# Kernel tuning notes

Measured on AMD Instinct MI355X. Metric: run time of the kernel, lower is better.

Reference implementation:

```python
import jax, jax.numpy as jnp
import numpy as np

N = 60000          # users
M = 40000          # items
NODES = N + M
D = 64             # embedding_dim
NLAYERS = 3        # layers = [64, 64, 64]
NNZ = 3_200_000    # nnz of L_I (avg degree 32)
B = 1024           # batch_size
NEG_SLOPE = 0.2


def setup_inputs() -> dict:
    key = jax.random.key(0)
    ks = jax.random.split(key, 12)
    edge_row = jax.random.randint(ks[0], (NNZ,), 0, NODES, dtype=jnp.int32)
    edge_col = jax.random.randint(ks[1], (NNZ,), 0, NODES, dtype=jnp.int32)
    # Laplacian values are small positive normalized weights
    edge_val = jax.random.uniform(ks[2], (NNZ,), dtype=jnp.float32) * (1.0 / 32.0)
    embed_user = jax.random.normal(ks[3], (N, D), dtype=jnp.float32) * 0.1
    embed_item = jax.random.normal(ks[4], (M, D), dtype=jnp.float32) * 0.1
    W1 = jax.random.normal(ks[5], (NLAYERS, D, D), dtype=jnp.float32) * 0.1
    W2 = jax.random.normal(ks[6], (NLAYERS, D, D), dtype=jnp.float32) * 0.1
    b1 = jax.random.normal(ks[7], (NLAYERS, 1, D), dtype=jnp.float32) * 0.1
    b2 = jax.random.normal(ks[8], (NLAYERS, 1, D), dtype=jnp.float32) * 0.1
    sampled_users = jax.random.randint(ks[9], (B,), 0, N, dtype=jnp.int32)
    observed_items_idx = jax.random.randint(ks[10], (B,), 0, M, dtype=jnp.int32)
    unobserved_items_idx = jax.random.randint(ks[11], (B,), 0, M, dtype=jnp.int32)
    return {
        "edge_row": edge_row, "edge_col": edge_col, "edge_val": edge_val,
        "embed_user": embed_user, "embed_item": embed_item,
        "W1": W1, "W2": W2, "b1": b1, "b2": b2,
        "sampled_users": sampled_users,
        "observed_items_idx": observed_items_idx,
        "unobserved_items_idx": unobserved_items_idx,
    }


def _spmm(row, col, val, x):
    # sparse (NODES x NODES) @ dense (NODES x D) via gather + segment-sum
    return jax.ops.segment_sum(val[:, None] * x[col], row, num_segments=NODES)


def reference(edge_row, edge_col, edge_val, embed_user, embed_item,
              W1, W2, b1, b2,
              sampled_users, observed_items_idx, unobserved_items_idx):
    x = jnp.concatenate([embed_user, embed_item], axis=0)  # (NODES, D)
    reprs = [x]
    for i in range(NLAYERS):
        lie = _spmm(edge_row, edge_col, edge_val, x)        # L_I @ E
        left = lie @ W1[i] + b1[i]
        right = (x * lie) @ W2[i] + b2[i]
        x = jax.nn.leaky_relu(left + right, negative_slope=NEG_SLOPE)
        reprs.append(x)
    final_reprs = jnp.concatenate(reprs, axis=1)            # (NODES, D*(NLAYERS+1))
    users_, items_ = final_reprs[:N], final_reprs[N:]
    return (users_[sampled_users],
            items_[observed_items_idx],
            items_[unobserved_items_idx])
```

## Files before the change

kernel.cpp:

```cpp
#include <hip/hip_runtime.h>

#define NN    60000
#define NODES 100000
#define DD    64
#define NNZ   3200000
#define BB    1024
#define NEG   0.2f
#define RPB   196
#define NBUCK 511
#define EPB   8192
#define NPB   ((NNZ + EPB - 1) / EPB)
#define CAP   7000
#define BCAP  7168
#define NSEG  13
#define KEYN  (NSEG * RPB)
#define SPB   (KEYN + 1)

__global__ __launch_bounds__(256) void k_init_x(const float* __restrict__ eu,
                                                const float* __restrict__ ei,
                                                float* __restrict__ x,
                                                int* __restrict__ gcur) {
    int i = blockIdx.x * 256 + threadIdx.x;
    if (i < NBUCK) gcur[i] = i * CAP;
    const int TOT = NODES * DD / 4;
    if (i >= TOT) return;
    const int UE = NN * DD / 4;
    float4 v = (i < UE) ? ((const float4*)eu)[i] : ((const float4*)ei)[i - UE];
    ((float4*)x)[i] = v;
}

__global__ __launch_bounds__(512) void k_place(const int* __restrict__ row,
                                               const int* __restrict__ col,
                                               const float* __restrict__ val,
                                               int* __restrict__ gcur,
                                               int2* __restrict__ bulk) {
    __shared__ int rows_l[EPB];
    __shared__ unsigned short perm[EPB];
    __shared__ int h[NBUCK], bloc[NBUCK], bcur[NBUCK], gseg[NBUCK];
    __shared__ int sc[512];
    int t = threadIdx.x;
    if (t < NBUCK) h[t] = 0;
    __syncthreads();
    int base = blockIdx.x * EPB;
    int n = min(EPB, NNZ - base);
    for (int k = t; k < n; k += 512) {
        int r = row[base + k];
        rows_l[k] = r;
        atomicAdd(&h[r / RPB], 1);
    }
    __syncthreads();
    {
        int v = (t < NBUCK) ? h[t] : 0;
        sc[t] = v;
        __syncthreads();
        for (int off = 1; off < 512; off <<= 1) {
            int u = (t >= off) ? sc[t - off] : 0;
            __syncthreads();
            sc[t] += u;
            __syncthreads();
        }
        if (t < NBUCK) {
            int ex = sc[t] - v;
            bloc[t] = ex;
            bcur[t] = ex;
            gseg[t] = v ? atomicAdd(&gcur[t], v) : 0;
        }
    }
    __syncthreads();
    for (int k = t; k < n; k += 512) {
        int p = atomicAdd(&bcur[rows_l[k] / RPB], 1);
        perm[p] = (unsigned short)k;
    }
    __syncthreads();
    for (int j = t; j < n; j += 512) {
        int k = perm[j];
        int r = rows_l[k];
        int b = r / RPB;
        int addr = gseg[b] + (j - bloc[b]);
        bulk[addr] = make_int2(((r - b * RPB) << 17) | col[base + k],
                               __float_as_int(val[base + k]));
    }
}

__global__ __launch_bounds__(512) void k_csr(const int* __restrict__ gcur,
                                             int2* __restrict__ bulk,
                                             int* __restrict__ starts) {
    __shared__ int2 eds[BCAP];
    __shared__ int cnt[KEYN], pos[KEYN];
    __shared__ int part[512];
    int b = blockIdx.x, t = threadIdx.x;
    int lo = b * CAP;
    int n = gcur[b] - lo;
    for (int k = t; k < KEYN; k += 512) cnt[k] = 0;
    __syncthreads();
    for (int i = t; i < n; i += 512) {
        int2 ed = bulk[lo + i];
        eds[i] = ed;
        int lr = ed.x >> 17, c = ed.x & 0x1FFFF;
        atomicAdd(&cnt[(c >> 13) * RPB + lr], 1);
    }
    __syncthreads();
    int run = 0;
#pragma unroll
    for (int j = 0; j < 5; ++j) {
        int k = t * 5 + j;
        if (k < KEYN) { pos[k] = run; run += cnt[k]; }
    }
    part[t] = run;
    __syncthreads();
    for (int off = 1; off < 512; off <<= 1) {
        int u = (t >= off) ? part[t - off] : 0;
        __syncthreads();
        part[t] += u;
        __syncthreads();
    }
    int poff = part[t] - run;
#pragma unroll
    for (int j = 0; j < 5; ++j) {
        int k = t * 5 + j;
        if (k < KEYN) pos[k] += poff;
    }
    __syncthreads();
    for (int k = t; k < KEYN; k += 512) {
        starts[b * SPB + k] = lo + pos[k];
        cnt[k] = pos[k];
    }
    if (t == 0) starts[b * SPB + KEYN] = lo + n;
    __syncthreads();
    for (int i = t; i < n; i += 512) {
        int2 ed = eds[i];
        int lr = ed.x >> 17, c = ed.x & 0x1FFFF;
        int p = atomicAdd(&cnt[(c >> 13) * RPB + lr], 1);
        bulk[lo + p] = ed;
    }
}

__global__ __launch_bounds__(1024) void k_cspmm(const int* __restrict__ starts,
                                                const int2* __restrict__ cv,
                                                const float* __restrict__ x,
                                                float* __restrict__ lie) {
    __shared__ float acc[RPB * DD];
    int t = threadIdx.x, b = blockIdx.x;
    float4* av = (float4*)acc;
    for (int i = t; i < RPB * 16; i += 1024) av[i] = make_float4(0.f, 0.f, 0.f, 0.f);
    __syncthreads();
    int lane = t & 63;
    int wid = __builtin_amdgcn_readfirstlane(t >> 6);
    int r0 = (wid * RPB) >> 4;
    int r1 = ((wid + 1) * RPB) >> 4;
    int sb = b * SPB;
    for (int seg = 0; seg < NSEG; ++seg) {
        int s = starts[sb + seg * RPB + r0];
        int e = starts[sb + seg * RPB + r1];
        int cur = -1;
        float f = 0.f;
        int g = s;
        for (; g + 8 <= e; g += 8) {
            int2 ee[8];
#pragma unroll
            for (int j = 0; j < 8; ++j) ee[j] = cv[g + j];
            float xv[8];
#pragma unroll
            for (int j = 0; j < 8; ++j) xv[j] = x[(ee[j].x & 0x1FFFF) * DD + lane];
#pragma unroll
            for (int j = 0; j < 8; ++j) {
                int r = ee[j].x >> 17;
                if (r != cur) {
                    if (cur >= 0) acc[cur * DD + lane] += f;
                    cur = r; f = 0.f;
                }
                f = fmaf(__int_as_float(ee[j].y), xv[j], f);
            }
        }
        for (; g < e; ++g) {
            int2 ed = cv[g];
            float xg = x[(ed.x & 0x1FFFF) * DD + lane];
            int r = ed.x >> 17;
            if (r != cur) {
                if (cur >= 0) acc[cur * DD + lane] += f;
                cur = r; f = 0.f;
            }
            f = fmaf(__int_as_float(ed.y), xg, f);
        }
        if (cur >= 0) acc[cur * DD + lane] += f;
    }
    __syncthreads();
    int row0 = b * RPB;
    for (int i = t; i < RPB * 16; i += 1024) {
        int gr = row0 + (i >> 4);
        if (gr < NODES) ((float4*)lie)[gr * 16 + (i & 15)] = av[i];
    }
}

__global__ __launch_bounds__(256) void k_gemm(float* __restrict__ x,
                                              const float* __restrict__ lie,
                                              const float* __restrict__ W1,
                                              const float* __restrict__ W2,
                                              const float* __restrict__ b1,
                                              const float* __restrict__ b2) {
    __shared__ float A1[64 * 64];
    __shared__ float A2[64 * 64];
    __shared__ float Ws1[64 * 64];
    __shared__ float Ws2[64 * 64];

    const int t = threadIdx.x;
    const int row0 = blockIdx.x * 64;

    {
        const float4* w1v = (const float4*)W1;
        const float4* w2v = (const float4*)W2;
        float4* s1v = (float4*)Ws1;
        float4* s2v = (float4*)Ws2;
#pragma unroll
        for (int q = 0; q < 4; ++q) {
            s1v[q * 256 + t] = w1v[q * 256 + t];
            s2v[q * 256 + t] = w2v[q * 256 + t];
        }
    }
#pragma unroll
    for (int q = 0; q < 4; ++q) {
        int f4 = q * 256 + t;
        int rl = f4 >> 4;
        int c4 = f4 & 15;
        int gr = row0 + rl;
        float4 lv = make_float4(0.f, 0.f, 0.f, 0.f);
        float4 xv = make_float4(0.f, 0.f, 0.f, 0.f);
        if (gr < NODES) {
            lv = *(const float4*)&lie[gr * DD + c4 * 4];
            xv = *(const float4*)&x[gr * DD + c4 * 4];
        }
        int sg = c4 ^ (rl & 15);
        ((float4*)A1)[rl * 16 + sg] = lv;
        ((float4*)A2)[rl * 16 + sg] = make_float4(lv.x * xv.x, lv.y * xv.y,
                                                  lv.z * xv.z, lv.w * xv.w);
    }
    __syncthreads();

    const int tx = t & 15;
    const int ty = t >> 4;
    float bs[4];
    {
        float4 bb1 = *(const float4*)&b1[tx * 4];
        float4 bb2 = *(const float4*)&b2[tx * 4];
        bs[0] = bb1.x + bb2.x; bs[1] = bb1.y + bb2.y;
        bs[2] = bb1.z + bb2.z; bs[3] = bb1.w + bb2.w;
    }
    float acc[4][4];
#pragma unroll
    for (int i = 0; i < 4; ++i)
#pragma unroll
        for (int j = 0; j < 4; ++j) acc[i][j] = bs[j];

    for (int k4 = 0; k4 < 16; ++k4) {
        float4 a1[4], a2[4];
#pragma unroll
        for (int i = 0; i < 4; ++i) {
            int r = ty * 4 + i;
            int sg = k4 ^ (r & 15);
            a1[i] = ((const float4*)A1)[r * 16 + sg];
            a2[i] = ((const float4*)A2)[r * 16 + sg];
        }
#pragma unroll
        for (int kk = 0; kk < 4; ++kk) {
            float4 w1 = ((const float4*)Ws1)[(k4 * 4 + kk) * 16 + tx];
            float4 w2 = ((const float4*)Ws2)[(k4 * 4 + kk) * 16 + tx];
#pragma unroll
            for (int i = 0; i < 4; ++i) {
                float av1 = (&a1[i].x)[kk];
                float av2 = (&a2[i].x)[kk];
                acc[i][0] = fmaf(av1, w1.x, fmaf(av2, w2.x, acc[i][0]));
                acc[i][1] = fmaf(av1, w1.y, fmaf(av2, w2.y, acc[i][1]));
                acc[i][2] = fmaf(av1, w1.z, fmaf(av2, w2.z, acc[i][2]));
                acc[i][3] = fmaf(av1, w1.w, fmaf(av2, w2.w, acc[i][3]));
            }
        }
    }
#pragma unroll
    for (int i = 0; i < 4; ++i) {
        int gr = row0 + ty * 4 + i;
        if (gr < NODES) {
            float4 o;
            o.x = acc[i][0] >= 0.f ? acc[i][0] : NEG * acc[i][0];
            o.y = acc[i][1] >= 0.f ? acc[i][1] : NEG * acc[i][1];
            o.z = acc[i][2] >= 0.f ? acc[i][2] : NEG * acc[i][2];
            o.w = acc[i][3] >= 0.f ? acc[i][3] : NEG * acc[i][3];
            *(float4*)&x[gr * DD + tx * 4] = o;
        }
    }
}

__global__ __launch_bounds__(256) void k_gather(const float* __restrict__ x,
                                                const int* __restrict__ su,
                                                const int* __restrict__ oi,
                                                const int* __restrict__ ui,
                                                float* __restrict__ out, int layer) {
    int w    = (blockIdx.x * 256 + threadIdx.x) >> 6;
    int lane = threadIdx.x & 63;
    if (w >= 3 * BB) return;
    int g = w >> 10, b = w & 1023;
    int node = (g == 0) ? su[b] : (NN + ((g == 1) ? oi[b] : ui[b]));
    out[w * 256 + layer * 64 + lane] = x[node * DD + lane];
}

extern "C" void kernel_launch(void* const* d_in, const int* in_sizes, int n_in,
                              void* d_out, int out_size, void* d_ws, size_t ws_size,
                              hipStream_t stream) {
    const int*   edge_row = (const int*)d_in[0];
    const int*   edge_col = (const int*)d_in[1];
    const float* edge_val = (const float*)d_in[2];
    const float* eu = (const float*)d_in[3];
    const float* ei = (const float*)d_in[4];
    const float* W1 = (const float*)d_in[5];
    const float* W2 = (const float*)d_in[6];
    const float* b1 = (const float*)d_in[7];
    const float* b2 = (const float*)d_in[8];
    const int*   su = (const int*)d_in[9];
    const int*   oi = (const int*)d_in[10];
    const int*   ui = (const int*)d_in[11];
    float* out = (float*)d_out;

    float* x      = (float*)d_ws;
    float* lie    = x + NODES * DD;
    int2*  bulk   = (int2*)(lie + NODES * DD);
    int*   gcur   = (int*)(bulk + NBUCK * CAP);
    int*   starts = gcur + NBUCK + 1;

    k_init_x<<<(NODES * DD / 4 + 255) / 256, 256, 0, stream>>>(eu, ei, x, gcur);
    k_gather<<<(3 * BB * 64 + 255) / 256, 256, 0, stream>>>(x, su, oi, ui, out, 0);

    k_place<<<NPB, 512, 0, stream>>>(edge_row, edge_col, edge_val, gcur, bulk);
    k_csr<<<NBUCK, 512, 0, stream>>>(gcur, bulk, starts);

    for (int l = 0; l < 3; ++l) {
        k_cspmm<<<NBUCK, 1024, 0, stream>>>(starts, bulk, x, lie);
        k_gemm<<<(NODES + 63) / 64, 256, 0, stream>>>(x, lie,
                                                      W1 + l * 4096, W2 + l * 4096,
                                                      b1 + l * 64,  b2 + l * 64);
        k_gather<<<(3 * BB * 64 + 255) / 256, 256, 0, stream>>>(x, su, oi, ui, out, l + 1);
    }
}
```

Baseline: 524.2 us.

## Fuse SpMM with dense layer transform, ping-pong x buffers, software-pipeline gathers

Adds a fused kernel that keeps each block's L·E rows in shared memory and applies the W1/W2 transform, bias and leaky ReLU directly, skipping the intermediate lie write and re-read. x is now double-buffered so the fused kernel can read the old x while writing the new one. The SpMM inner loop is software-pipelined across two register sets so the next batch's edge loads and x gathers are issued before the current batch is consumed. Layer 1 still uses the separate SpMM plus GEMM path. The fused GEMM reads the weights from global memory per thread rather than staging them in shared memory, which may cost more in that phase.

```diff
diff --git a/kernel.cpp b/kernel.cpp
--- a/kernel.cpp
+++ b/kernel.cpp
@@ -135,9 +135,116 @@
     }
 }
 
+#define SPMM_BODY(XSRC, ACCDST)                                                  \
+    for (int seg = 0; seg < NSEG; ++seg) {                                       \
+        int s = starts[sb + seg * RPB + r0];                                     \
+        int e = starts[sb + seg * RPB + r1];                                     \
+        int cur = -1;                                                            \
+        float f = 0.f;                                                           \
+        int2 emA[8], emB[8];                                                     \
+        float xwA[8], xwB[8];                                                    \
+        int nb = (e - s) >> 3;                                                   \
+        if (nb > 0) {                                                            \
+            LDM(A, s) GTH(A, XSRC)                                               \
+            int ld = 1;                                                          \
+            for (;;) {                                                           \
+                if (ld < nb) { LDM(B, s + ld * 8) GTH(B, XSRC) ++ld; CNS(A, ACCDST) } \
+                else         { CNS(A, ACCDST) break; }                           \
+                if (ld < nb) { LDM(A, s + ld * 8) GTH(A, XSRC) ++ld; CNS(B, ACCDST) } \
+                else         { CNS(B, ACCDST) break; }                           \
+            }                                                                    \
+        }                                                                        \
+        for (int g = s + nb * 8; g < e; ++g) {                                   \
+            int2 ed = cv[g];                                                     \
+            float xg = XSRC[(ed.x & 0x1FFFF) * DD + lane];                       \
+            int r = ed.x >> 17;                                                  \
+            if (r != cur) {                                                      \
+                if (cur >= 0) ACCDST[cur * DD + lane] += f;                      \
+                cur = r; f = 0.f;                                                \
+            }                                                                    \
+            f = fmaf(__int_as_float(ed.y), xg, f);                               \
+        }                                                                        \
+        if (cur >= 0) ACCDST[cur * DD + lane] += f;                              \
+    }
+#define LDM(S, gg) { _Pragma("unroll") \
+    for (int j = 0; j < 8; ++j) em##S[j] = cv[(gg) + j]; }
+#define GTH(S, XSRC) { _Pragma("unroll") \
+    for (int j = 0; j < 8; ++j) xw##S[j] = XSRC[(em##S[j].x & 0x1FFFF) * DD + lane]; }
+#define CNS(S, ACCDST) { _Pragma("unroll") \
+    for (int j = 0; j < 8; ++j) { \
+        int r = em##S[j].x >> 17; \
+        if (r != cur) { if (cur >= 0) ACCDST[cur * DD + lane] += f; cur = r; f = 0.f; } \
+        f = fmaf(__int_as_float(em##S[j].y), xw##S[j], f); } }
+
+__global__ __launch_bounds__(1024) void k_fused(const int* __restrict__ starts,
+                                                const int2* __restrict__ cv,
+                                                const float* __restrict__ xs,
+                                                float* __restrict__ xd,
+                                                const float* __restrict__ W1,
+                                                const float* __restrict__ W2,
+                                                const float* __restrict__ b1,
+                                                const float* __restrict__ b2) {
+    __shared__ float acc[RPB * DD];
+    int t = threadIdx.x, b = blockIdx.x;
+    float4* av = (float4*)acc;
+    for (int i = t; i < RPB * 16; i += 1024) av[i] = make_float4(0.f, 0.f, 0.f, 0.f);
+    __syncthreads();
+    int lane = t & 63;
+    int wid = __builtin_amdgcn_readfirstlane(t >> 6);
+    int r0 = (wid * RPB) >> 4;
+    int r1 = ((wid + 1) * RPB) >> 4;
+    int sb = b * SPB;
+    SPMM_BODY(xs, acc)
+    __syncthreads();
+
+    {
+        const int row0 = b * RPB;
+        const int tx = t & 15;
+        const int ty = t >> 4;
+        const float4* w1v = (const float4*)W1;
+        const float4* w2v = (const float4*)W2;
+        float4 b1v = ((const float4*)b1)[tx];
+        float4 b2v = ((const float4*)b2)[tx];
+        float4 bb = make_float4(b1v.x + b2v.x, b1v.y + b2v.y,
+                                b1v.z + b2v.z, b1v.w + b2v.w);
+        int nr = (ty < RPB - 192) ? 4 : 3;
+        for (int i = 0; i < nr; ++i) {
+            int lr = ty + i * 64;
+            int gr = row0 + lr;
+            bool live = (gr < NODES);
+            float4 o = bb;
+            const float4* lrow = (const float4*)&acc[lr * DD];
+            const float4* xrow = (const float4*)&xs[(live ? gr : 0) * DD];
+#pragma unroll 2
+            for (int k4 = 0; k4 < 16; ++k4) {
+                float4 l4 = lrow[k4];
+                float4 x4 = xrow[k4];
+#pragma unroll
+                for (int kk = 0; kk < 4; ++kk) {
+                    float lk = (&l4.x)[kk];
+                    float ak = lk * (&x4.x)[kk];
+                    float4 w1r = w1v[(k4 * 4 + kk) * 16 + tx];
+                    float4 w2r = w2v[(k4 * 4 + kk) * 16 + tx];
+                    o.x = fmaf(lk, w1r.x, fmaf(ak, w2r.x, o.x));
+                    o.y = fmaf(lk, w1r.y, fmaf(ak, w2r.y, o.y));
+                    o.z = fmaf(lk, w1r.z, fmaf(ak, w2r.z, o.z));
+                    o.w = fmaf(lk, w1r.w, fmaf(ak, w2r.w, o.w));
+                }
+            }
+            if (live) {
+                o.x = o.x >= 0.f ? o.x : NEG * o.x;
+                o.y = o.y >= 0.f ? o.y : NEG * o.y;
+                o.z = o.z >= 0.f ? o.z : NEG * o.z;
+                o.w = o.w >= 0.f ? o.w : NEG * o.w;
+                ((float4*)xd)[gr * 16 + tx] = o;
+            }
+        }
+    }
+}
+
 __global__ __launch_bounds__(1024) void k_cspmm(const int* __restrict__ starts,
                                                 const int2* __restrict__ cv,
-                                                const float* __restrict__ x,
+                                                const float* __restrict__ xs,
                                                 float* __restrict__ lie) {
     __shared__ float acc[RPB * DD];
     int t = threadIdx.x, b = blockIdx.x;
@@ -149,41 +256,7 @@
     int r0 = (wid * RPB) >> 4;
     int r1 = ((wid + 1) * RPB) >> 4;
     int sb = b * SPB;
-    for (int seg = 0; seg < NSEG; ++seg) {
-        int s = starts[sb + seg * RPB + r0];
-        int e = starts[sb + seg * RPB + r1];
-        int cur = -1;
-        float f = 0.f;
-        int g = s;
-        for (; g + 8 <= e; g += 8) {
-            int2 ee[8];
-#pragma unroll
-            for (int j = 0; j < 8; ++j) ee[j] = cv[g + j];
-            float xv[8];
-#pragma unroll
-            for (int j = 0; j < 8; ++j) xv[j] = x[(ee[j].x & 0x1FFFF) * DD + lane];
-#pragma unroll
-            for (int j = 0; j < 8; ++j) {
-                int r = ee[j].x >> 17;
-                if (r != cur) {
-                    if (cur >= 0) acc[cur * DD + lane] += f;
-                    cur = r; f = 0.f;
-                }
-                f = fmaf(__int_as_float(ee[j].y), xv[j], f);
-            }
-        }
-        for (; g < e; ++g) {
-            int2 ed = cv[g];
-            float xg = x[(ed.x & 0x1FFFF) * DD + lane];
-            int r = ed.x >> 17;
-            if (r != cur) {
-                if (cur >= 0) acc[cur * DD + lane] += f;
-                cur = r; f = 0.f;
-            }
-            f = fmaf(__int_as_float(ed.y), xg, f);
-        }
-        if (cur >= 0) acc[cur * DD + lane] += f;
-    }
+    SPMM_BODY(xs, acc)
     __syncthreads();
     int row0 = b * RPB;
     for (int i = t; i < RPB * 16; i += 1024) {
@@ -191,13 +264,17 @@
         if (gr < NODES) ((float4*)lie)[gr * 16 + (i & 15)] = av[i];
     }
 }
-
-__global__ __launch_bounds__(256) void k_gemm(float* __restrict__ x,
-                                              const float* __restrict__ lie,
-                                              const float* __restrict__ W1,
-                                              const float* __restrict__ W2,
-                                              const float* __restrict__ b1,
-                                              const float* __restrict__ b2) {
+#undef LDM
+#undef GTH
+#undef CNS
+#undef SPMM_BODY
+
+__global__ __launch_bounds__(256) void k_gemm_pp(const float* __restrict__ x_in,
+                                                 float* __restrict__ liex,
+                                                 const float* __restrict__ W1,
+                                                 const float* __restrict__ W2,
+                                                 const float* __restrict__ b1,
+                                                 const float* __restrict__ b2) {
     __shared__ float A1[64 * 64];
     __shared__ float A2[64 * 64];
     __shared__ float Ws1[64 * 64];
@@ -226,8 +303,8 @@
         float4 lv = make_float4(0.f, 0.f, 0.f, 0.f);
         float4 xv = make_float4(0.f, 0.f, 0.f, 0.f);
         if (gr < NODES) {
-            lv = *(const float4*)&lie[gr * DD + c4 * 4];
-            xv = *(const float4*)&x[gr * DD + c4 * 4];
+            lv = *(const float4*)&liex[gr * DD + c4 * 4];
+            xv = *(const float4*)&x_in[gr * DD + c4 * 4];
         }
         int sg = c4 ^ (rl & 15);
         ((float4*)A1)[rl * 16 + sg] = lv;
@@ -284,7 +361,7 @@
             o.y = acc[i][1] >= 0.f ? acc[i][1] : NEG * acc[i][1];
             o.z = acc[i][2] >= 0.f ? acc[i][2] : NEG * acc[i][2];
             o.w = acc[i][3] >= 0.f ? acc[i][3] : NEG * acc[i][3];
-            *(float4*)&x[gr * DD + tx * 4] = o;
+            *(float4*)&liex[gr * DD + tx * 4] = o;
         }
     }
 }
@@ -319,23 +396,33 @@
     const int*   ui = (const int*)d_in[11];
     float* out = (float*)d_out;
 
-    float* x      = (float*)d_ws;
-    float* lie    = x + NODES * DD;
-    int2*  bulk   = (int2*)(lie + NODES * DD);
+    float* xa     = (float*)d_ws;
+    float* xb     = xa + NODES * DD;
+    int2*  bulk   = (int2*)(xb + NODES * DD);
     int*   gcur   = (int*)(bulk + NBUCK * CAP);
     int*   starts = gcur + NBUCK + 1;
 
-    k_init_x<<<(NODES * DD / 4 + 255) / 256, 256, 0, stream>>>(eu, ei, x, gcur);
-    k_gather<<<(3 * BB * 64 + 255) / 256, 256, 0, stream>>>(x, su, oi, ui, out, 0);
+    k_init_x<<<(NODES * DD / 4 + 255) / 256, 256, 0, stream>>>(eu, ei, xa, gcur);
+    k_gather<<<(3 * BB * 64 + 255) / 256, 256, 0, stream>>>(xa, su, oi, ui, out, 0);
 
     k_place<<<NPB, 512, 0, stream>>>(edge_row, edge_col, edge_val, gcur, bulk);
     k_csr<<<NBUCK, 512, 0, stream>>>(gcur, bulk, starts);
 
+    const float* xsrc = xa;
+    float*       xdst = xb;
     for (int l = 0; l < 3; ++l) {
-        k_cspmm<<<NBUCK, 1024, 0, stream>>>(starts, bulk, x, lie);
-        k_gemm<<<(NODES + 63) / 64, 256, 0, stream>>>(x, lie,
-                                                      W1 + l * 4096, W2 + l * 4096,
-                                                      b1 + l * 64,  b2 + l * 64);
-        k_gather<<<(3 * BB * 64 + 255) / 256, 256, 0, stream>>>(x, su, oi, ui, out, l + 1);
-    }
-}
+        if (l == 1) {
+            k_cspmm<<<NBUCK, 1024, 0, stream>>>(starts, bulk, xsrc, xdst);
+            k_gemm_pp<<<(NODES + 63) / 64, 256, 0, stream>>>(xsrc, xdst,
+                                                             W1 + l * 4096, W2 + l * 4096,
+                                                             b1 + l * 64,  b2 + l * 64);
+        } else {
+            k_fused<<<NBUCK, 1024, 0, stream>>>(starts, bulk, xsrc, xdst,
+                                                W1 + l * 4096, W2 + l * 4096,
+                                                b1 + l * 64,  b2 + l * 64);
+        }
+        k_gather<<<(3 * BB * 64 + 255) / 256, 256, 0, stream>>>(xdst, su, oi, ui,
+                                                                out, l + 1);
+        const float* tmp = xsrc; xsrc = xdst; xdst = (float*)tmp;
+    }
+}
```

Result: slower. 632.2 us (+20.6%).
